# Kernel tuning notes

Hardware: AMD Instinct MI355X
Metric: run time of the kernel (lower is better)

## Reference

```python
import jax, jax.numpy as jnp
import numpy as np


def _adj(p):
    # p: [B,N,C] -> W = exp(-pairwise squared distance), fully dense (incl. self loops)
    sq = jnp.sum(p * p, axis=-1, keepdims=True)            # [B,N,1]
    d = sq - 2.0 * jnp.einsum('bnc,bmc->bnm', p, p) + jnp.swapaxes(sq, 1, 2)
    return jnp.exp(-d)


def _cheb_lap(W):
    # PyG ChebConv norm with sym normalization, lambda_max=2: L_hat = L - I = -D^{-1/2} W D^{-1/2}
    dinv = jax.lax.rsqrt(jnp.sum(W, axis=-1))              # [B,N]
    return -(dinv[:, :, None] * W * dinv[:, None, :])


def _reg_lap(W):
    # get_laplacian(sym) after remove_self_loops: L = I - D'^{-1/2} W' D'^{-1/2}, W' = W with zero diag
    N = W.shape[1]
    eye = jnp.eye(N, dtype=W.dtype)
    W0 = W * (1.0 - eye)
    dinv = jax.lax.rsqrt(jnp.sum(W0, axis=-1))
    return eye - dinv[:, :, None] * W0 * dinv[:, None, :]


def _cheb(x, Lhat, Wk, b):
    # Chebyshev recursion: Z0=x, Z1=L_hat x, Zk = 2 L_hat Z_{k-1} - Z_{k-2}
    # x: [B,N,Cin], Lhat: [B,N,N], Wk: [K,Cin,Cout]
    Z0 = x
    out = jnp.einsum('bni,io->bno', Z0, Wk[0])
    if Wk.shape[0] > 1:
        Z1 = jnp.einsum('bnm,bmi->bni', Lhat, x)
        out = out + jnp.einsum('bni,io->bno', Z1, Wk[1])
        for k in range(2, Wk.shape[0]):
            Z2 = 2.0 * jnp.einsum('bnm,bmi->bni', Lhat, Z1) - Z0
            out = out + jnp.einsum('bni,io->bno', Z2, Wk[k])
            Z0, Z1 = Z1, Z2
    return out + b


def _reg(out, L):
    # ||out^T L out||_F, block-diagonal L -> sum over batch blocks
    M = jnp.einsum('bnc,bnm,bmd->cd', out, L, out)
    return jnp.linalg.norm(M)


def setup_inputs() -> dict:
    key = jax.random.key(0)
    ks = jax.random.split(key, 16)
    B, N = 16, 1024
    s = 0.05
    return {
        'x': jax.random.normal(ks[0], (B, N, 6), dtype=jnp.float32),
        'batch': jnp.repeat(jnp.arange(B, dtype=jnp.int64 if jax.config.jax_enable_x64 else jnp.int32), N),
        'batch_size': B,
        'nr_points': N,
        'w1': jax.random.normal(ks[1], (6, 6, 128), dtype=jnp.float32) * s,
        'b1': jnp.zeros((128,), dtype=jnp.float32),
        'w2': jax.random.normal(ks[2], (5, 128, 512), dtype=jnp.float32) * s,
        'b2': jnp.zeros((512,), dtype=jnp.float32),
        'w3': jax.random.normal(ks[3], (3, 512, 1024), dtype=jnp.float32) * s,
        'b3': jnp.zeros((1024,), dtype=jnp.float32),
        'fw1': jax.random.normal(ks[4], (1024, 512), dtype=jnp.float32) * s,
        'fb1': jnp.zeros((512,), dtype=jnp.float32),
        'fw2': jax.random.normal(ks[5], (512, 128), dtype=jnp.float32) * s,
        'fb2': jnp.zeros((128,), dtype=jnp.float32),
        'fw3': jax.random.normal(ks[6], (128, 10), dtype=jnp.float32) * s,
        'fb3': jnp.zeros((10,), dtype=jnp.float32),
    }


def reference(x, batch, batch_size, nr_points, w1, b1, w2, b2, w3, b3,
              fw1, fb1, fw2, fb2, fw3, fb3):
    sg = jax.lax.stop_gradient
    # reshape of x happens inside torch.no_grad -> input to conv1 is detached
    h = sg(x)
    W1 = sg(_adj(x))
    out = jax.nn.relu(_cheb(h, _cheb_lap(W1), w1, b1))            # [B,N,128]
    r1 = sg(_reg(out, _reg_lap(W1)))
    W2 = sg(_adj(out))
    out = jax.nn.relu(_cheb(out, sg(_cheb_lap(W2)), w2, b2))      # [B,N,512]
    r2 = sg(_reg(out, _reg_lap(W2)))
    W3 = sg(_adj(out))
    out = jax.nn.relu(_cheb(out, sg(_cheb_lap(W3)), w3, b3))      # [B,N,1024]
    r3 = sg(_reg(out, _reg_lap(W3)))
    pooled = jnp.max(out, axis=1)                                  # MaxPool1d over points
    h = jax.nn.relu(pooled @ fw1 + fb1)
    h = jax.nn.relu(h @ fw2 + fb2)
    logits = h @ fw3 + fb3
    return logits, r1, r2, r3
```

## Files before the change

kernel.cpp:

```cpp
#include <hip/hip_runtime.h>

#define BB 16
#define NN 1024
#define LDT 16384

typedef float4 f4;
typedef __attribute__((ext_vector_type(8))) short bf16x8;
typedef __attribute__((ext_vector_type(4))) float f32x4;

__device__ __forceinline__ unsigned f2b1(float f) {
    unsigned u = __builtin_bit_cast(unsigned, f);
    return (u + 0x7fffu + ((u >> 16) & 1u)) >> 16;
}
__device__ __forceinline__ float b2f1(unsigned s) {
    unsigned u = (s & 0xffffu) << 16;
    return __builtin_bit_cast(float, u);
}

#define SW(r, k) ((r) * 64 + ((k) ^ (((((r) & 7) ^ (((r) >> 3) & 7))) << 3)))

__device__ __forceinline__ void gload16(const unsigned short* g, short* l) {
    __builtin_amdgcn_global_load_lds(
        (const __attribute__((address_space(1))) unsigned int*)g,
        (__attribute__((address_space(3))) unsigned int*)l, 16, 0, 0);
}

__device__ __forceinline__ float wave_sum(float v) {
    #pragma unroll
    for (int m = 32; m >= 1; m >>= 1) v += __shfl_xor(v, m);
    return v;
}
__device__ __forceinline__ float wave_max(float v) {
    #pragma unroll
    for (int m = 32; m >= 1; m >>= 1) v = fmaxf(v, __shfl_xor(v, m));
    return v;
}

__device__ __forceinline__ void stage_tr(short* T, const unsigned short* src,
                                         size_t col_base, int c0, int Cvalid, int tid) {
    #pragma unroll
    for (int n = 0; n < 2; n++) {
        int q = n * 256 + tid;
        int p = q >> 4, h = q & 15;
        int cg = c0 + 2 * p;
        uint4 r0 = make_uint4(0, 0, 0, 0), r1 = make_uint4(0, 0, 0, 0);
        if (cg < Cvalid)     r0 = *(const uint4*)&src[(size_t)cg * LDT + col_base + 8 * h];
        if (cg + 1 < Cvalid) r1 = *(const uint4*)&src[(size_t)(cg + 1) * LDT + col_base + 8 * h];
        const unsigned* a0 = (const unsigned*)&r0;
        const unsigned* a1 = (const unsigned*)&r1;
        #pragma unroll
        for (int e = 0; e < 8; e++) {
            unsigned lo = (e & 1) ? (a0[e >> 1] >> 16) : (a0[e >> 1] & 0xffffu);
            unsigned hi = (e & 1) ? (a1[e >> 1] >> 16) : (a1[e >> 1] & 0xffffu);
            int r = 8 * h + e;
            *(unsigned*)&T[SW(r, 2 * p)] = lo | (hi << 16);
        }
    }
}

__global__ void xt_prep_kernel(const float* __restrict__ x, short* __restrict__ xh,
                               short* __restrict__ xl) {
    int m = blockIdx.x * 256 + threadIdx.x;
    #pragma unroll
    for (int c = 0; c < 8; c++) {
        float v = (c < 6) ? x[(size_t)m * 6 + c] : 0.f;
        unsigned h = f2b1(v);
        unsigned l = f2b1(v - b2f1(h));
        xh[(size_t)c * LDT + m] = (short)h;
        xl[(size_t)c * LDT + m] = (short)l;
    }
}

__global__ void wtt_prep_kernel(const float* __restrict__ Wk, short* __restrict__ WtT,
                                int Kp64, int KpValid, int CpadM1, int shift, int Cin, int Cout) {
    int idx = blockIdx.x * 256 + threadIdx.x;
    if (idx >= Cout * Kp64) return;
    int co = idx / Kp64, kk = idx - co * Kp64;
    int c = kk & CpadM1;
    float val = 0.f;
    if (kk < KpValid && c < Cin)
        val = Wk[((size_t)(kk >> shift) * Cin + c) * Cout + co];
    WtT[(size_t)co * Kp64 + kk] = (short)f2b1(val);
}

__global__ void wtrans_kernel(const float* __restrict__ Wt, float* __restrict__ WtT,
                              int K, int O) {
    int idx = blockIdx.x * 256 + threadIdx.x;
    if (idx >= K * O) return;
    int o = idx / K, k = idx - o * K;
    WtT[idx] = Wt[(size_t)k * O + o];
}

__global__ void scale_sc_kernel(const short* __restrict__ src, const float* __restrict__ coeff,
                                short* __restrict__ dst, int total8) {
    int q = blockIdx.x * 256 + threadIdx.x;
    if (q >= total8) return;
    size_t base = (size_t)q * 8;
    int m8 = (int)(base & (LDT - 1));
    uint4 v = *(const uint4*)&((const unsigned short*)src)[base];
    f4 c0 = *(const f4*)&coeff[m8];
    f4 c1 = *(const f4*)&coeff[m8 + 4];
    const float* cp0 = (const float*)&c0;
    const float* cp1 = (const float*)&c1;
    unsigned* vp = (unsigned*)&v;
    #pragma unroll
    for (int e = 0; e < 4; e++) {
        float se0 = (e < 2) ? cp0[2 * e] : cp1[2 * e - 4];
        float se1 = (e < 2) ? cp0[2 * e + 1] : cp1[2 * e - 3];
        vp[e] = f2b1(b2f1(vp[e]) * se0) | (f2b1(b2f1(vp[e] >> 16) * se1) << 16);
    }
    *(uint4*)&((unsigned short*)dst)[base] = v;
}

__global__ __launch_bounds__(256)
void xpose_kernel(const short* __restrict__ H, const short* __restrict__ L,
                  int Cvalid, int CR, short* __restrict__ XRh, short* __restrict__ XRl) {
    __shared__ short Th[128 * 64], Tl[128 * 64];
    int tid = threadIdx.x;
    int m0 = blockIdx.x * 128, c0 = blockIdx.y * 64;
    stage_tr(Th, (const unsigned short*)H, m0, c0, Cvalid, tid);
    stage_tr(Tl, (const unsigned short*)L, m0, c0, Cvalid, tid);
    __syncthreads();
    #pragma unroll
    for (int n = 0; n < 4; n++) {
        int q = n * 256 + tid;
        int r = q >> 3, j = q & 7;
        int g = (r & 7) ^ ((r >> 3) & 7);
        *(uint4*)&XRh[(size_t)(m0 + r) * CR + c0 + 8 * j] = *(const uint4*)&Th[r * 64 + 8 * (j ^ g)];
        *(uint4*)&XRl[(size_t)(m0 + r) * CR + c0 + 8 * j] = *(const uint4*)&Tl[r * 64 + 8 * (j ^ g)];
    }
}

__global__ void sqt_part_kernel(const short* __restrict__ H, const short* __restrict__ L,
                                int C, float* __restrict__ dst) {
    int m = blockIdx.x * 256 + threadIdx.x;
    int cb = blockIdx.y * 128;
    int ce = min(cb + 128, C);
    const unsigned short* Hp = (const unsigned short*)H;
    const unsigned short* Lp = (const unsigned short*)L;
    float s = 0.f;
    for (int c = cb; c < ce; c++) {
        float v = b2f1(Hp[(size_t)c * LDT + m]) + b2f1(Lp[(size_t)c * LDT + m]);
        s += v * v;
    }
    dst[(size_t)blockIdx.y * LDT + m] = s;
}
__global__ void sqt_red_kernel(const float* __restrict__ part, int NC, float* __restrict__ sq) {
    int m = blockIdx.x * 256 + threadIdx.x;
    float s = 0.f;
    for (int y = 0; y < NC; y++) s += part[(size_t)y * LDT + m];
    sq[m] = s;
}

__global__ __launch_bounds__(256)
void adj_mfma_kernel(const short* __restrict__ XRh, const short* __restrict__ XRl,
                     int ck64, int CR, const float* __restrict__ sq,
                     short* __restrict__ Wb, float* __restrict__ Wpart,
                     float* __restrict__ diagW) {
    __shared__ short Ah[128 * 64], Al[128 * 64], Bh[128 * 64], Bl[128 * 64];
    __shared__ float jpart[128][2];
    int tid = threadIdx.x, lane = tid & 63, w = tid >> 6;
    int wj = w >> 1, wi = w & 1;
    int b = blockIdx.z, i0 = blockIdx.x * 128, j0 = blockIdx.y * 128;
    size_t bo = (size_t)b * NN;
    f32x4 acc[4][4] = {};
    const unsigned short* Hp = (const unsigned short*)XRh;
    const unsigned short* Lp = (const unsigned short*)XRl;
    int rr = lane >> 3, jj = lane & 7;
    size_t offI[4], offJ[4];
    #pragma unroll
    for (int m = 0; m < 4; m++) {
        int s = w + m * 4;
        int jc = jj ^ rr ^ (s & 7);
        offI[m] = (size_t)(bo + i0 + 8 * s + rr) * CR + 8 * jc;
        offJ[m] = (size_t)(bo + j0 + 8 * s + rr) * CR + 8 * jc;
    }
    for (int t = 0; t < ck64; t++) {
        int c0 = t * 64;
        #pragma unroll
        for (int m = 0; m < 4; m++) {
            int s512 = (w + m * 4) * 512;
            gload16(Hp + offI[m] + c0, Ah + s512);
            gload16(Lp + offI[m] + c0, Al + s512);
            gload16(Hp + offJ[m] + c0, Bh + s512);
            gload16(Lp + offJ[m] + c0, Bl + s512);
        }
        __syncthreads();
        int la = lane & 15;
        #pragma unroll
        for (int ks = 0; ks < 2; ks++) {
            int kb = ks * 32 + (lane >> 4) * 8;
            bf16x8 jh[4], jl[4], ih[4], il[4];
            #pragma unroll
            for (int f = 0; f < 4; f++) {
                int jr = wj * 64 + f * 16 + la;
                jh[f] = *(const bf16x8*)&Bh[SW(jr, kb)];
                jl[f] = *(const bf16x8*)&Bl[SW(jr, kb)];
                int ir = wi * 64 + f * 16 + la;
                ih[f] = *(const bf16x8*)&Ah[SW(ir, kb)];
                il[f] = *(const bf16x8*)&Al[SW(ir, kb)];
            }
            #pragma unroll
            for (int fq = 0; fq < 4; fq++)
                #pragma unroll
                for (int fi = 0; fi < 4; fi++) {
                    acc[fq][fi] = __builtin_amdgcn_mfma_f32_16x16x32_bf16(jh[fq], ih[fi], acc[fq][fi], 0, 0, 0);
                    acc[fq][fi] = __builtin_amdgcn_mfma_f32_16x16x32_bf16(jh[fq], il[fi], acc[fq][fi], 0, 0, 0);
                    acc[fq][fi] = __builtin_amdgcn_mfma_f32_16x16x32_bf16(jl[fq], ih[fi], acc[fq][fi], 0, 0, 0);
                }
        }
        __syncthreads();
    }
    const float* sqb = sq + bo;
    unsigned short* Wout = (unsigned short*)Wb + bo * NN;
    float si_[4];
    int iloc[4];
    #pragma unroll
    for (int fi = 0; fi < 4; fi++) {
        iloc[fi] = i0 + wi * 64 + fi * 16 + (lane & 15);
        si_[fi] = sqb[iloc[fi]];
    }
    #pragma unroll
    for (int fq = 0; fq < 4; fq++) {
        int jb = j0 + wj * 64 + fq * 16 + (lane >> 4) * 4;
        #pragma unroll
        for (int r = 0; r < 4; r++) {
            int j = jb + r;
            float sj = sqb[j];
            float p = 0.f;
            #pragma unroll
            for (int fi = 0; fi < 4; fi++) {
                float val = __expf(2.f * ((const float*)&acc[fq][fi])[r] - si_[fi] - sj);
                Wout[(size_t)j * NN + iloc[fi]] = (unsigned short)f2b1(val);
                if (iloc[fi] == j) diagW[bo + j] = val;
                else p += val;
            }
            p += __shfl_xor(p, 1); p += __shfl_xor(p, 2);
            p += __shfl_xor(p, 4); p += __shfl_xor(p, 8);
            if ((lane & 15) == 0)
                jpart[wj * 64 + fq * 16 + (lane >> 4) * 4 + r][wi] = p;
        }
    }
    __syncthreads();
    if (tid < 128)
        Wpart[(size_t)blockIdx.x * (BB * NN) + bo + j0 + tid] = jpart[tid][0] + jpart[tid][1];
}

__global__ void reduce_prep_kernel(const float* __restrict__ Wpart, const float* __restrict__ diagW,
                                   float* dinv, float* dinvP, float* cA1, float* cA2, float* cAV) {
    int idx = blockIdx.x * 256 + threadIdx.x;
    float s = 0.f;
    #pragma unroll
    for (int x = 0; x < 8; x++) s += Wpart[(size_t)x * (BB * NN) + idx];
    float d = diagW[idx];
    float dv = rsqrtf(s + d);
    float dp = rsqrtf(s);
    dinv[idx] = dv; dinvP[idx] = dp;
    cA1[idx] = -dv; cA2[idx] = -2.f * dv; cAV[idx] = -dp;
}

template<bool HAS_PREV, bool SKIP_DIAG, bool WRITE_SC>
__global__ __launch_bounds__(512)
void wgemm2_kernel(const short* __restrict__ W, const short* __restrict__ Bsc,
                   const float* __restrict__ cAvec, float prevSign,
                   const short* __restrict__ PrevT, const float* __restrict__ scVec,
                   short* __restrict__ DstT, short* __restrict__ DstSc, int Cvalid) {
    __shared__ short As[128 * 64], Bs[128 * 64];
    int tid = threadIdx.x, lane = tid & 63, w = tid >> 6;
    int wcc = w >> 2, wii = w & 3;
    int b = blockIdx.z, i0 = blockIdx.x * 128, c0 = blockIdx.y * 128;
    size_t bo = (size_t)b * NN;
    const unsigned short* Wp = (const unsigned short*)W + bo * NN;
    const unsigned short* Bp = (const unsigned short*)Bsc;
    int rr = lane >> 3, jj = lane & 7;
    int sA = w, sB = w + 8;
    int jc = jj ^ rr ^ (w & 7);
    const unsigned short* aR0 = Wp + (size_t)(i0 + 8 * sA + rr) * NN + 8 * jc;
    const unsigned short* aR1 = Wp + (size_t)(i0 + 8 * sB + rr) * NN + 8 * jc;
    const unsigned short* bR0 = Bp + (size_t)(c0 + 8 * sA + rr) * LDT + bo + 8 * jc;
    const unsigned short* bR1 = Bp + (size_t)(c0 + 8 * sB + rr) * LDT + bo + 8 * jc;
    short* aL0 = As + sA * 512; short* aL1 = As + sB * 512;
    short* bL0 = Bs + sA * 512; short* bL1 = Bs + sB * 512;
    f32x4 acc[4][2] = {};
    for (int k0 = 0; k0 < NN; k0 += 64) {
        gload16(aR0 + k0, aL0);
        gload16(aR1 + k0, aL1);
        gload16(bR0 + k0, bL0);
        gload16(bR1 + k0, bL1);
        __syncthreads();
        if (SKIP_DIAG) {
            if (k0 == i0 || k0 == i0 + 64) {
                if (tid < 64) As[SW((k0 - i0) + tid, tid)] = 0;
                __syncthreads();
            }
        }
        int la = lane & 15;
        #pragma unroll
        for (int ks = 0; ks < 2; ks++) {
            int kb = ks * 32 + (lane >> 4) * 8;
            bf16x8 ac[4], bi[2];
            #pragma unroll
            for (int f = 0; f < 4; f++) ac[f] = *(const bf16x8*)&Bs[SW(wcc * 64 + f * 16 + la, kb)];
            #pragma unroll
            for (int f = 0; f < 2; f++) bi[f] = *(const bf16x8*)&As[SW(wii * 32 + f * 16 + la, kb)];
            #pragma unroll
            for (int fq = 0; fq < 4; fq++)
                #pragma unroll
                for (int fi = 0; fi < 2; fi++)
                    acc[fq][fi] = __builtin_amdgcn_mfma_f32_16x16x32_bf16(ac[fq], bi[fi], acc[fq][fi], 0, 0, 0);
        }
        __syncthreads();
    }
    const unsigned short* Pp = (const unsigned short*)PrevT;
    unsigned short* Dp = (unsigned short*)DstT;
    unsigned short* Sp = (unsigned short*)DstSc;
    #pragma unroll
    for (int fi = 0; fi < 2; fi++) {
        int i = i0 + wii * 32 + fi * 16 + (lane & 15);
        float ca = cAvec[bo + i];
        float sc = WRITE_SC ? scVec[bo + i] : 0.f;
        #pragma unroll
        for (int fq = 0; fq < 4; fq++) {
            int cb = c0 + wcc * 64 + fq * 16 + (lane >> 4) * 4;
            const float* av = (const float*)&acc[fq][fi];
            #pragma unroll
            for (int r = 0; r < 4; r++) {
                int c = cb + r;
                if (c < Cvalid) {
                    float v = ca * av[r];
                    if (HAS_PREV) v += prevSign * b2f1(Pp[(size_t)c * LDT + bo + i]);
                    Dp[(size_t)c * LDT + bo + i] = (unsigned short)f2b1(v);
                    if (WRITE_SC) Sp[(size_t)c * LDT + bo + i] = (unsigned short)f2b1(v * sc);
                }
            }
        }
    }
}

__global__ __launch_bounds__(512)
void fgemm_mfma_kernel(const short* __restrict__ A0T, const short* __restrict__ ZrT,
                       const short* __restrict__ WtT, int Kp64, int KpValid, int Cpad,
                       const float* __restrict__ bias,
                       short* __restrict__ OutH, short* __restrict__ OutL) {
    __shared__ short As[128 * 64], Bs[128 * 64];
    int tid = threadIdx.x, lane = tid & 63, w = tid >> 6;
    int wco = w >> 2, wm = w & 3;
    int m0 = blockIdx.x * 128, co0 = blockIdx.y * 128;
    const unsigned short* A0 = (const unsigned short*)A0T;
    const unsigned short* Zr = (const unsigned short*)ZrT;
    const unsigned short* Wt = (const unsigned short*)WtT;
    f32x4 acc[4][2] = {};
    for (int kk0 = 0; kk0 < Kp64; kk0 += 64) {
        {
            int p = tid >> 4, h = tid & 15;
            int kg0 = kk0 + 2 * p;
            uint4 r0 = make_uint4(0, 0, 0, 0), r1 = make_uint4(0, 0, 0, 0);
            if (kg0 < KpValid) {
                const unsigned short* s0 = (kg0 < Cpad) ? (A0 + (size_t)kg0 * LDT)
                                                        : (Zr + (size_t)(kg0 - Cpad) * LDT);
                r0 = *(const uint4*)&s0[m0 + 8 * h];
            }
            if (kg0 + 1 < KpValid) {
                int kg1 = kg0 + 1;
                const unsigned short* s1 = (kg1 < Cpad) ? (A0 + (size_t)kg1 * LDT)
                                                        : (Zr + (size_t)(kg1 - Cpad) * LDT);
                r1 = *(const uint4*)&s1[m0 + 8 * h];
            }
            const unsigned* a0 = (const unsigned*)&r0;
            const unsigned* a1 = (const unsigned*)&r1;
            #pragma unroll
            for (int e = 0; e < 8; e++) {
                unsigned lo = (e & 1) ? (a0[e >> 1] >> 16) : (a0[e >> 1] & 0xffffu);
                unsigned hi = (e & 1) ? (a1[e >> 1] >> 16) : (a1[e >> 1] & 0xffffu);
                *(unsigned*)&As[SW(8 * h + e, 2 * p)] = lo | (hi << 16);
            }
        }
        #pragma unroll
        for (int n = 0; n < 2; n++) {
            int q = n * 512 + tid;
            int r = q >> 3, k8 = (q & 7) * 8;
            uint4 v = *(const uint4*)&Wt[(size_t)(co0 + r) * Kp64 + kk0 + k8];
            *(uint4*)&Bs[SW(r, k8)] = v;
        }
        __syncthreads();
        int la = lane & 15;
        #pragma unroll
        for (int ks = 0; ks < 2; ks++) {
            int kb = ks * 32 + (lane >> 4) * 8;
            bf16x8 ac[4], bm[2];
            #pragma unroll
            for (int f = 0; f < 4; f++) ac[f] = *(const bf16x8*)&Bs[SW(wco * 64 + f * 16 + la, kb)];
            #pragma unroll
            for (int f = 0; f < 2; f++) bm[f] = *(const bf16x8*)&As[SW(wm * 32 + f * 16 + la, kb)];
            #pragma unroll
            for (int fq = 0; fq < 4; fq++)
                #pragma unroll
                for (int fi = 0; fi < 2; fi++)
                    acc[fq][fi] = __builtin_amdgcn_mfma_f32_16x16x32_bf16(ac[fq], bm[fi], acc[fq][fi], 0, 0, 0);
        }
        __syncthreads();
    }
    unsigned short* OH = (unsigned short*)OutH;
    unsigned short* OL = (unsigned short*)OutL;
    #pragma unroll
    for (int fi = 0; fi < 2; fi++) {
        int m = m0 + wm * 32 + fi * 16 + (lane & 15);
        #pragma unroll
        for (int fq = 0; fq < 4; fq++) {
            int cb = co0 + wco * 64 + fq * 16 + (lane >> 4) * 4;
            const float* av = (const float*)&acc[fq][fi];
            #pragma unroll
            for (int r = 0; r < 4; r++) {
                int co = cb + r;
                float v = av[r] + bias[co];
                v = v > 0.f ? v : 0.f;
                unsigned ph = f2b1(v);
                unsigned pl = f2b1(v - b2f1(ph));
                OH[(size_t)co * LDT + m] = (unsigned short)ph;
                OL[(size_t)co * LDT + m] = (unsigned short)pl;
            }
        }
    }
}

__global__ __launch_bounds__(256)
void mgemm_mfma_kernel(const short* __restrict__ XT, const short* __restrict__ VT,
                       float* __restrict__ Mpart, int Cout, int kChunk) {
    __shared__ short As[128 * 64], Bs[128 * 64];
    int tid = threadIdx.x, lane = tid & 63, w = tid >> 6;
    int wcj = w >> 1, wci = w & 1;
    int ci0 = blockIdx.x * 128, cj0 = blockIdx.y * 128;
    int kStart = blockIdx.z * kChunk;
    const unsigned short* Xp = (const unsigned short*)XT + (size_t)ci0 * LDT;
    const unsigned short* Vp = (const unsigned short*)VT + (size_t)cj0 * LDT;
    int rr = lane >> 3, jj = lane & 7;
    const unsigned short* aB[4];
    const unsigned short* bB[4];
    short* aL[4]; short* bL[4];
    #pragma unroll
    for (int n = 0; n < 4; n++) {
        int s = w + n * 4;
        int jc = jj ^ rr ^ (s & 7);
        aB[n] = Xp + (size_t)(8 * s + rr) * LDT + 8 * jc;
        bB[n] = Vp + (size_t)(8 * s + rr) * LDT + 8 * jc;
        aL[n] = As + s * 512; bL[n] = Bs + s * 512;
    }
    f32x4 acc[4][4] = {};
    for (int k0 = kStart; k0 < kStart + kChunk; k0 += 64) {
        #pragma unroll
        for (int n = 0; n < 4; n++) {
            gload16(aB[n] + k0, aL[n]);
            gload16(bB[n] + k0, bL[n]);
        }
        __syncthreads();
        int la = lane & 15;
        #pragma unroll
        for (int ks = 0; ks < 2; ks++) {
            int kb = ks * 32 + (lane >> 4) * 8;
            bf16x8 aj[4], bi[4];
            #pragma unroll
            for (int f = 0; f < 4; f++) {
                aj[f] = *(const bf16x8*)&Bs[SW(wcj * 64 + f * 16 + la, kb)];
                bi[f] = *(const bf16x8*)&As[SW(wci * 64 + f * 16 + la, kb)];
            }
            #pragma unroll
            for (int fq = 0; fq < 4; fq++)
                #pragma unroll
                for (int fi = 0; fi < 4; fi++)
                    acc[fq][fi] = __builtin_amdgcn_mfma_f32_16x16x32_bf16(aj[fq], bi[fi], acc[fq][fi], 0, 0, 0);
        }
        __syncthreads();
    }
    float* pt = Mpart + (size_t)blockIdx.z * Cout * Cout;
    #pragma unroll
    for (int fq = 0; fq < 4; fq++) {
        int cjb = cj0 + wcj * 64 + fq * 16 + (lane >> 4) * 4;
        #pragma unroll
        for (int fi = 0; fi < 4; fi++) {
            int ci = ci0 + wci * 64 + fi * 16 + (lane & 15);
            const float* av = (const float*)&acc[fq][fi];
            #pragma unroll
            for (int r = 0; r < 4; r++)
                pt[(size_t)(cjb + r) * Cout + ci] = av[r];
        }
    }
}

__global__ void fro1_kernel(const float* __restrict__ part, int nElem, int splitk,
                            float* __restrict__ blockSS) {
    int tid = threadIdx.x;
    float ss = 0.f;
    for (int idx = blockIdx.x * 256 + tid; idx < nElem; idx += 1024 * 256) {
        float s = 0.f;
        for (int z = 0; z < splitk; z++) s += part[(size_t)z * nElem + idx];
        ss += s * s;
    }
    __shared__ float red[256];
    red[tid] = ss; __syncthreads();
    for (int m = 128; m >= 1; m >>= 1) { if (tid < m) red[tid] += red[tid + m]; __syncthreads(); }
    if (tid == 0) blockSS[blockIdx.x] = red[0];
}
__global__ void fro2_kernel(const float* __restrict__ blockSS, float* __restrict__ outp) {
    int tid = threadIdx.x;
    float s = 0.f;
    for (int i = tid; i < 1024; i += 256) s += blockSS[i];
    __shared__ float red[256];
    red[tid] = s; __syncthreads();
    for (int m = 128; m >= 1; m >>= 1) { if (tid < m) red[tid] += red[tid + m]; __syncthreads(); }
    if (tid == 0) *outp = sqrtf(red[0]);
}

__global__ void pool_kernel(const short* __restrict__ H, const short* __restrict__ L,
                            float* __restrict__ out) {
    int wave = threadIdx.x >> 6, lane = threadIdx.x & 63;
    int r = blockIdx.x * 4 + wave;
    int co = r >> 4, b = r & 15;
    const unsigned short* h = (const unsigned short*)H + (size_t)co * LDT + b * NN;
    const unsigned short* l = (const unsigned short*)L + (size_t)co * LDT + b * NN;
    float m = -1e30f;
    #pragma unroll
    for (int it = 0; it < 2; it++) {
        int n8 = (it * 64 + lane) * 8;
        uint4 vh = *(const uint4*)&h[n8];
        uint4 vl = *(const uint4*)&l[n8];
        const unsigned* hp = (const unsigned*)&vh;
        const unsigned* lp = (const unsigned*)&vl;
        #pragma unroll
        for (int e = 0; e < 4; e++) {
            m = fmaxf(m, b2f1(hp[e]) + b2f1(lp[e]));
            m = fmaxf(m, b2f1(hp[e] >> 16) + b2f1(lp[e] >> 16));
        }
    }
    m = wave_max(m);
    if (lane == 0) out[b * 1024 + co] = m;
}

__global__ void fc_kernel(const float* __restrict__ in, const float* __restrict__ WtT,
                          const float* __restrict__ bias, float* __restrict__ out,
                          int K, int O, int doRelu) {
    int wave = threadIdx.x >> 6, lane = threadIdx.x & 63;
    int idx = blockIdx.x * 4 + wave;
    if (idx >= 16 * O) return;
    int b = idx / O, o = idx - b * O;
    const float* ib = in + (size_t)b * K;
    const float* wr = WtT + (size_t)o * K;
    float s = 0.f;
    for (int k = lane * 4; k < K; k += 256) {
        f4 a = *(const f4*)&ib[k];
        f4 wv = *(const f4*)&wr[k];
        s += a.x * wv.x + a.y * wv.y + a.z * wv.z + a.w * wv.w;
    }
    s = wave_sum(s);
    if (lane == 0) {
        s += bias[o];
        if (doRelu) s = fmaxf(s, 0.f);
        out[(size_t)b * O + o] = s;
    }
}

extern "C" void kernel_launch(void* const* d_in, const int* in_sizes, int n_in,
                              void* d_out, int out_size, void* d_ws, size_t ws_size,
                              hipStream_t stream) {
    const float* x   = (const float*)d_in[0];
    const float* w1  = (const float*)d_in[4];
    const float* b1  = (const float*)d_in[5];
    const float* w2  = (const float*)d_in[6];
    const float* b2  = (const float*)d_in[7];
    const float* w3  = (const float*)d_in[8];
    const float* b3  = (const float*)d_in[9];
    const float* fw1 = (const float*)d_in[10];
    const float* fb1 = (const float*)d_in[11];
    const float* fw2 = (const float*)d_in[12];
    const float* fb2 = (const float*)d_in[13];
    const float* fw3 = (const float*)d_in[14];
    const float* fb3 = (const float*)d_in[15];
    float* out = (float*)d_out;

    char* ws = (char*)d_ws;
    size_t off = 0;
    auto alloc = [&](size_t bytes) -> void* {
        void* p = ws + off; off += (bytes + 255) & ~(size_t)255; return p;
    };
    short* Wbuf = (short*)alloc((size_t)BB * NN * NN * 2);
    short* Zbuf = (short*)alloc((size_t)1024 * LDT * 2);
    short* ZSc  = (short*)alloc((size_t)1024 * LDT * 2);
    short* Z0Sc = (short*)alloc((size_t)512 * LDT * 2);
    short* XRh  = (short*)alloc((size_t)512 * LDT * 2);
    short* XRl  = (short*)alloc((size_t)512 * LDT * 2);
    short* o1H  = (short*)alloc((size_t)128 * LDT * 2);
    short* o1L  = (short*)alloc((size_t)128 * LDT * 2);
    short* o2H  = (short*)alloc((size_t)512 * LDT * 2);
    short* o2L  = (short*)alloc((size_t)512 * LDT * 2);
    short* o3H  = (short*)alloc((size_t)1024 * LDT * 2);
    short* o3L  = (short*)alloc((size_t)1024 * LDT * 2);
    short* xTh  = (short*)alloc((size_t)8 * LDT * 2);
    short* xTl  = (short*)alloc((size_t)8 * LDT * 2);
    short* WtT  = (short*)alloc((size_t)1024 * 1536 * 2);
    float* fwT1 = (float*)alloc((size_t)512 * 1024 * 4);
    float* fwT2 = (float*)alloc((size_t)128 * 512 * 4);
    float* fwT3 = (float*)alloc((size_t)10 * 128 * 4);
    float* sqpart = (float*)alloc((size_t)8 * LDT * 4);
    float* Wpart  = (float*)alloc((size_t)8 * BB * NN * 4);
    float* diagW  = (float*)alloc(BB * NN * 4);
    float* sq    = (float*)alloc(BB * NN * 4);
    float* dinv  = (float*)alloc(BB * NN * 4);
    float* dinvP = (float*)alloc(BB * NN * 4);
    float* cA1   = (float*)alloc(BB * NN * 4);
    float* cA2   = (float*)alloc(BB * NN * 4);
    float* cAV   = (float*)alloc(BB * NN * 4);
    float* pooled= (float*)alloc(BB * 1024 * 4);
    float* h1    = (float*)alloc(BB * 512 * 4);
    float* h2    = (float*)alloc(BB * 128 * 4);
    float* blockSS = (float*)alloc(1024 * 4);
    float* Mpart = (float*)Wbuf;
    (void)ws_size; (void)in_sizes; (void)n_in; (void)out_size;

    struct Layer {
        const short *XTh, *XTl;
        int C, K, Cpad, shift, Kp64, KpValid, Cout, splitk, rIdx;
        const float *Wk, *bk;
        short *OutH, *OutL;
    };
    Layer L[3] = {
        { xTh, xTl, 8,   6, 8,   3, 64,   48,   128,  64, 160, w1, b1, o1H, o1L },
        { o1H, o1L, 128, 5, 128, 7, 640,  640,  512,  32, 161, w2, b2, o2H, o2L },
        { o2H, o2L, 512, 3, 512, 9, 1536, 1536, 1024, 8,  162, w3, b3, o3H, o3L },
    };

    xt_prep_kernel<<<LDT / 256, 256, 0, stream>>>(x, xTh, xTl);
    wtrans_kernel<<<(1024 * 512 + 255) / 256, 256, 0, stream>>>(fw1, fwT1, 1024, 512);
    wtrans_kernel<<<(512 * 128 + 255) / 256, 256, 0, stream>>>(fw2, fwT2, 512, 128);
    wtrans_kernel<<<(128 * 10 + 255) / 256, 256, 0, stream>>>(fw3, fwT3, 128, 10);

    for (int l = 0; l < 3; l++) {
        const Layer& P = L[l];
        int NC = (P.C + 127) / 128;
        int CR = (P.Cpad < 64) ? 64 : P.Cpad;
        wtt_prep_kernel<<<(P.Cout * P.Kp64 + 255) / 256, 256, 0, stream>>>(
            P.Wk, WtT, P.Kp64, P.KpValid, P.Cpad - 1, P.shift, (l == 0) ? 6 : P.C, P.Cout);
        sqt_part_kernel<<<dim3(LDT / 256, NC), 256, 0, stream>>>(P.XTh, P.XTl, P.C, sqpart);
        sqt_red_kernel<<<LDT / 256, 256, 0, stream>>>(sqpart, NC, sq);
        xpose_kernel<<<dim3(LDT / 128, CR / 64), 256, 0, stream>>>(
            P.XTh, P.XTl, P.Cpad, CR, XRh, XRl);
        adj_mfma_kernel<<<dim3(8, 8, BB), 256, 0, stream>>>(XRh, XRl, CR / 64, CR, sq,
                                                            Wbuf, Wpart, diagW);
        reduce_prep_kernel<<<BB * NN / 256, 256, 0, stream>>>(Wpart, diagW, dinv, dinvP, cA1, cA2, cAV);

        scale_sc_kernel<<<(P.Cpad * LDT / 8 + 255) / 256, 256, 0, stream>>>(
            P.XTh, dinv, Z0Sc, P.Cpad * LDT / 8);

        int cT = (P.Cpad + 127) / 128;
        auto sliceR = [&](int k) -> short* { return Zbuf + (size_t)(k - 1) * P.Cpad * LDT; };
        auto sliceS = [&](int k) -> short* { return ZSc  + (size_t)(k - 1) * P.Cpad * LDT; };
        if (P.K > 2)
            wgemm2_kernel<false, false, true><<<dim3(8, cT, BB), 512, 0, stream>>>(
                Wbuf, Z0Sc, cA1, 0.f, (const short*)nullptr, dinv, sliceR(1), sliceS(1), P.Cpad);
        else
            wgemm2_kernel<false, false, false><<<dim3(8, cT, BB), 512, 0, stream>>>(
                Wbuf, Z0Sc, cA1, 0.f, (const short*)nullptr, dinv, sliceR(1), (short*)nullptr, P.Cpad);
        for (int k = 2; k < P.K; k++) {
            const short* prevT = (k == 2) ? P.XTh : sliceR(k - 2);
            if (k < P.K - 1)
                wgemm2_kernel<true, false, true><<<dim3(8, cT, BB), 512, 0, stream>>>(
                    Wbuf, sliceS(k - 1), cA2, -1.f, prevT, dinv, sliceR(k), sliceS(k), P.Cpad);
            else
                wgemm2_kernel<true, false, false><<<dim3(8, cT, BB), 512, 0, stream>>>(
                    Wbuf, sliceS(k - 1), cA2, -1.f, prevT, dinv, sliceR(k), (short*)nullptr, P.Cpad);
        }
        fgemm_mfma_kernel<<<dim3(LDT / 128, P.Cout / 128), 512, 0, stream>>>(
            P.XTh, Zbuf, WtT, P.Kp64, P.KpValid, P.Cpad, P.bk, P.OutH, P.OutL);
        scale_sc_kernel<<<(P.Cout * LDT / 8 + 255) / 256, 256, 0, stream>>>(
            P.OutH, dinvP, ZSc, P.Cout * LDT / 8);
        wgemm2_kernel<true, true, false><<<dim3(8, P.Cout / 128, BB), 512, 0, stream>>>(
            Wbuf, ZSc, cAV, 1.f, P.OutH, dinvP, Zbuf, (short*)nullptr, P.Cout);
        int kChunk = LDT / P.splitk;
        mgemm_mfma_kernel<<<dim3(P.Cout / 128, P.Cout / 128, P.splitk), 256, 0, stream>>>(
            P.OutH, Zbuf, Mpart, P.Cout, kChunk);
        fro1_kernel<<<1024, 256, 0, stream>>>(Mpart, P.Cout * P.Cout, P.splitk, blockSS);
        fro2_kernel<<<1, 256, 0, stream>>>(blockSS, out + P.rIdx);
    }
    pool_kernel<<<16384 / 4, 256, 0, stream>>>(o3H, o3L, pooled);
    fc_kernel<<<(16 * 512 + 3) / 4, 256, 0, stream>>>(pooled, fwT1, fb1, h1, 1024, 512, 1);
    fc_kernel<<<(16 * 128 + 3) / 4, 256, 0, stream>>>(h1, fwT2, fb2, h2, 512, 128, 1);
    fc_kernel<<<(16 * 10 + 3) / 4, 256, 0, stream>>>(h2, fwT3, fb3, out, 128, 10, 0);
}
```

Before: 962.8 us.

## Use 64-row W tiles for narrow layers and prefetch A in fgemm

Adds an XB template parameter to the Laplacian GEMM kernel so layers with at most 128 channels use 64-row tiles. This doubles the block count where the grid was small (8x1x16) and should improve occupancy. Separately, fgemm now loads its weight tile asynchronously into LDS via global_load_lds and prefetches the next A tile into registers during compute, overlapping global loads with MFMA work. The costs are more re-reads of the B operand with smaller tiles and extra register pressure from the prefetch.

```diff
diff --git a/kernel.cpp b/kernel.cpp
--- a/kernel.cpp
+++ b/kernel.cpp
@@ -259,37 +259,38 @@
     cA1[idx] = -dv; cA2[idx] = -2.f * dv; cAV[idx] = -dp;
 }
 
-template<bool HAS_PREV, bool SKIP_DIAG, bool WRITE_SC>
+template<bool HAS_PREV, bool SKIP_DIAG, bool WRITE_SC, int XB>
 __global__ __launch_bounds__(512)
 void wgemm2_kernel(const short* __restrict__ W, const short* __restrict__ Bsc,
                    const float* __restrict__ cAvec, float prevSign,
                    const short* __restrict__ PrevT, const float* __restrict__ scVec,
                    short* __restrict__ DstT, short* __restrict__ DstSc, int Cvalid) {
-    __shared__ short As[128 * 64], Bs[128 * 64];
+    __shared__ short As[XB * 64], Bs[128 * 64];
+    constexpr int NFI = XB / 64;
     int tid = threadIdx.x, lane = tid & 63, w = tid >> 6;
     int wcc = w >> 2, wii = w & 3;
-    int b = blockIdx.z, i0 = blockIdx.x * 128, c0 = blockIdx.y * 128;
+    int b = blockIdx.z, i0 = blockIdx.x * XB, c0 = blockIdx.y * 128;
     size_t bo = (size_t)b * NN;
     const unsigned short* Wp = (const unsigned short*)W + bo * NN;
     const unsigned short* Bp = (const unsigned short*)Bsc;
     int rr = lane >> 3, jj = lane & 7;
-    int sA = w, sB = w + 8;
     int jc = jj ^ rr ^ (w & 7);
-    const unsigned short* aR0 = Wp + (size_t)(i0 + 8 * sA + rr) * NN + 8 * jc;
-    const unsigned short* aR1 = Wp + (size_t)(i0 + 8 * sB + rr) * NN + 8 * jc;
-    const unsigned short* bR0 = Bp + (size_t)(c0 + 8 * sA + rr) * LDT + bo + 8 * jc;
-    const unsigned short* bR1 = Bp + (size_t)(c0 + 8 * sB + rr) * LDT + bo + 8 * jc;
-    short* aL0 = As + sA * 512; short* aL1 = As + sB * 512;
-    short* bL0 = Bs + sA * 512; short* bL1 = Bs + sB * 512;
-    f32x4 acc[4][2] = {};
+    const unsigned short* aR0 = Wp + (size_t)(i0 + 8 * w + rr) * NN + 8 * jc;
+    const unsigned short* aR1 = Wp + (size_t)(i0 + 8 * ((XB == 128) ? w + 8 : w) + rr) * NN + 8 * jc;
+    const unsigned short* bR0 = Bp + (size_t)(c0 + 8 * w + rr) * LDT + bo + 8 * jc;
+    const unsigned short* bR1 = Bp + (size_t)(c0 + 8 * (w + 8) + rr) * LDT + bo + 8 * jc;
+    short* aL0 = As + w * 512;
+    short* aL1 = As + ((XB == 128) ? w + 8 : w) * 512;
+    short* bL0 = Bs + w * 512; short* bL1 = Bs + (w + 8) * 512;
+    f32x4 acc[4][NFI] = {};
     for (int k0 = 0; k0 < NN; k0 += 64) {
         gload16(aR0 + k0, aL0);
-        gload16(aR1 + k0, aL1);
+        if (XB == 128) gload16(aR1 + k0, aL1);
         gload16(bR0 + k0, bL0);
         gload16(bR1 + k0, bL1);
         __syncthreads();
         if (SKIP_DIAG) {
-            if (k0 == i0 || k0 == i0 + 64) {
+            if (k0 >= i0 && k0 < i0 + XB) {
                 if (tid < 64) As[SW((k0 - i0) + tid, tid)] = 0;
                 __syncthreads();
             }
@@ -298,15 +299,15 @@
         #pragma unroll
         for (int ks = 0; ks < 2; ks++) {
             int kb = ks * 32 + (lane >> 4) * 8;
-            bf16x8 ac[4], bi[2];
+            bf16x8 ac[4], bi[NFI];
             #pragma unroll
             for (int f = 0; f < 4; f++) ac[f] = *(const bf16x8*)&Bs[SW(wcc * 64 + f * 16 + la, kb)];
             #pragma unroll
-            for (int f = 0; f < 2; f++) bi[f] = *(const bf16x8*)&As[SW(wii * 32 + f * 16 + la, kb)];
+            for (int f = 0; f < NFI; f++) bi[f] = *(const bf16x8*)&As[SW(wii * (XB / 4) + f * 16 + la, kb)];
             #pragma unroll
             for (int fq = 0; fq < 4; fq++)
                 #pragma unroll
-                for (int fi = 0; fi < 2; fi++)
+                for (int fi = 0; fi < NFI; fi++)
                     acc[fq][fi] = __builtin_amdgcn_mfma_f32_16x16x32_bf16(ac[fq], bi[fi], acc[fq][fi], 0, 0, 0);
         }
         __syncthreads();
@@ -315,8 +316,8 @@
     unsigned short* Dp = (unsigned short*)DstT;
     unsigned short* Sp = (unsigned short*)DstSc;
     #pragma unroll
-    for (int fi = 0; fi < 2; fi++) {
-        int i = i0 + wii * 32 + fi * 16 + (lane & 15);
+    for (int fi = 0; fi < NFI; fi++) {
+        int i = i0 + wii * (XB / 4) + fi * 16 + (lane & 15);
         float ca = cAvec[bo + i];
         float sc = WRITE_SC ? scVec[bo + i] : 0.f;
         #pragma unroll
@@ -349,25 +350,34 @@
     const unsigned short* A0 = (const unsigned short*)A0T;
     const unsigned short* Zr = (const unsigned short*)ZrT;
     const unsigned short* Wt = (const unsigned short*)WtT;
+    int rr = lane >> 3, jj = lane & 7;
+    int jcB = jj ^ rr ^ (w & 7);
+    const unsigned short* bB0 = Wt + (size_t)(co0 + 8 * w + rr) * Kp64 + 8 * jcB;
+    const unsigned short* bB1 = Wt + (size_t)(co0 + 8 * (w + 8) + rr) * Kp64 + 8 * jcB;
+    short* bL0 = Bs + w * 512; short* bL1 = Bs + (w + 8) * 512;
+    int p = tid >> 4, h = tid & 15;
+    uint4 ra0, ra1;
+    auto loadA = [&](int kk0) {
+        int kg0 = kk0 + 2 * p;
+        ra0 = make_uint4(0, 0, 0, 0); ra1 = make_uint4(0, 0, 0, 0);
+        if (kg0 < KpValid) {
+            const unsigned short* s0 = (kg0 < Cpad) ? (A0 + (size_t)kg0 * LDT)
+                                                    : (Zr + (size_t)(kg0 - Cpad) * LDT);
+            ra0 = *(const uint4*)&s0[m0 + 8 * h];
+        }
+        if (kg0 + 1 < KpValid) {
+            int kg1 = kg0 + 1;
+            const unsigned short* s1 = (kg1 < Cpad) ? (A0 + (size_t)kg1 * LDT)
+                                                    : (Zr + (size_t)(kg1 - Cpad) * LDT);
+            ra1 = *(const uint4*)&s1[m0 + 8 * h];
+        }
+    };
     f32x4 acc[4][2] = {};
+    loadA(0);
     for (int kk0 = 0; kk0 < Kp64; kk0 += 64) {
         {
-            int p = tid >> 4, h = tid & 15;
-            int kg0 = kk0 + 2 * p;
-            uint4 r0 = make_uint4(0, 0, 0, 0), r1 = make_uint4(0, 0, 0, 0);
-            if (kg0 < KpValid) {
-                const unsigned short* s0 = (kg0 < Cpad) ? (A0 + (size_t)kg0 * LDT)
-                                                        : (Zr + (size_t)(kg0 - Cpad) * LDT);
-                r0 = *(const uint4*)&s0[m0 + 8 * h];
-            }
-            if (kg0 + 1 < KpValid) {
-                int kg1 = kg0 + 1;
-                const unsigned short* s1 = (kg1 < Cpad) ? (A0 + (size_t)kg1 * LDT)
-                                                        : (Zr + (size_t)(kg1 - Cpad) * LDT);
-                r1 = *(const uint4*)&s1[m0 + 8 * h];
-            }
-            const unsigned* a0 = (const unsigned*)&r0;
-            const unsigned* a1 = (const unsigned*)&r1;
+            const unsigned* a0 = (const unsigned*)&ra0;
+            const unsigned* a1 = (const unsigned*)&ra1;
             #pragma unroll
             for (int e = 0; e < 8; e++) {
                 unsigned lo = (e & 1) ? (a0[e >> 1] >> 16) : (a0[e >> 1] & 0xffffu);
@@ -375,14 +385,10 @@
                 *(unsigned*)&As[SW(8 * h + e, 2 * p)] = lo | (hi << 16);
             }
         }
-        #pragma unroll
-        for (int n = 0; n < 2; n++) {
-            int q = n * 512 + tid;
-            int r = q >> 3, k8 = (q & 7) * 8;
-            uint4 v = *(const uint4*)&Wt[(size_t)(co0 + r) * Kp64 + kk0 + k8];
-            *(uint4*)&Bs[SW(r, k8)] = v;
-        }
+        gload16(bB0 + kk0, bL0);
+        gload16(bB1 + kk0, bL1);
         __syncthreads();
+        if (kk0 + 64 < Kp64) loadA(kk0 + 64);
         int la = lane & 15;
         #pragma unroll
         for (int ks = 0; ks < 2; ks++) {
@@ -650,29 +656,45 @@
             P.XTh, dinv, Z0Sc, P.Cpad * LDT / 8);
 
         int cT = (P.Cpad + 127) / 128;
+        bool sm = (P.Cpad <= 128);
         auto sliceR = [&](int k) -> short* { return Zbuf + (size_t)(k - 1) * P.Cpad * LDT; };
         auto sliceS = [&](int k) -> short* { return ZSc  + (size_t)(k - 1) * P.Cpad * LDT; };
-        if (P.K > 2)
-            wgemm2_kernel<false, false, true><<<dim3(8, cT, BB), 512, 0, stream>>>(
-                Wbuf, Z0Sc, cA1, 0.f, (const short*)nullptr, dinv, sliceR(1), sliceS(1), P.Cpad);
-        else
-            wgemm2_kernel<false, false, false><<<dim3(8, cT, BB), 512, 0, stream>>>(
-                Wbuf, Z0Sc, cA1, 0.f, (const short*)nullptr, dinv, sliceR(1), (short*)nullptr, P.Cpad);
+        if (P.K > 2) {
+            if (sm) wgemm2_kernel<false, false, true, 64><<<dim3(NN / 64, cT, BB), 512, 0, stream>>>(
+                        Wbuf, Z0Sc, cA1, 0.f, (const short*)nullptr, dinv, sliceR(1), sliceS(1), P.Cpad);
+            else    wgemm2_kernel<false, false, true, 128><<<dim3(NN / 128, cT, BB), 512, 0, stream>>>(
+                        Wbuf, Z0Sc, cA1, 0.f, (const short*)nullptr, dinv, sliceR(1), sliceS(1), P.Cpad);
+        } else {
+            if (sm) wgemm2_kernel<false, false, false, 64><<<dim3(NN / 64, cT, BB), 512, 0, stream>>>(
+                        Wbuf, Z0Sc, cA1, 0.f, (const short*)nullptr, dinv, sliceR(1), (short*)nullptr, P.Cpad);
+            else    wgemm2_kernel<false, false, false, 128><<<dim3(NN / 128, cT, BB), 512, 0, stream>>>(
+                        Wbuf, Z0Sc, cA1, 0.f, (const short*)nullptr, dinv, sliceR(1), (short*)nullptr, P.Cpad);
+        }
         for (int k = 2; k < P.K; k++) {
             const short* prevT = (k == 2) ? P.XTh : sliceR(k - 2);
-            if (k < P.K - 1)
-                wgemm2_kernel<true, false, true><<<dim3(8, cT, BB), 512, 0, stream>>>(
-                    Wbuf, sliceS(k - 1), cA2, -1.f, prevT, dinv, sliceR(k), sliceS(k), P.Cpad);
-            else
-                wgemm2_kernel<true, false, false><<<dim3(8, cT, BB), 512, 0, stream>>>(
-                    Wbuf, sliceS(k - 1), cA2, -1.f, prevT, dinv, sliceR(k), (short*)nullptr, P.Cpad);
+            if (k < P.K - 1) {
+                if (sm) wgemm2_kernel<true, false, true, 64><<<dim3(NN / 64, cT, BB), 512, 0, stream>>>(
+                            Wbuf, sliceS(k - 1), cA2, -1.f, prevT, dinv, sliceR(k), sliceS(k), P.Cpad);
+                else    wgemm2_kernel<true, false, true, 128><<<dim3(NN / 128, cT, BB), 512, 0, stream>>>(
+                            Wbuf, sliceS(k - 1), cA2, -1.f, prevT, dinv, sliceR(k), sliceS(k), P.Cpad);
+            } else {
+                if (sm) wgemm2_kernel<true, false, false, 64><<<dim3(NN / 64, cT, BB), 512, 0, stream>>>(
+                            Wbuf, sliceS(k - 1), cA2, -1.f, prevT, dinv, sliceR(k), (short*)nullptr, P.Cpad);
+                else    wgemm2_kernel<true, false, false, 128><<<dim3(NN / 128, cT, BB), 512, 0, stream>>>(
+                            Wbuf, sliceS(k - 1), cA2, -1.f, prevT, dinv, sliceR(k), (short*)nullptr, P.Cpad);
+            }
         }
         fgemm_mfma_kernel<<<dim3(LDT / 128, P.Cout / 128), 512, 0, stream>>>(
             P.XTh, Zbuf, WtT, P.Kp64, P.KpValid, P.Cpad, P.bk, P.OutH, P.OutL);
         scale_sc_kernel<<<(P.Cout * LDT / 8 + 255) / 256, 256, 0, stream>>>(
             P.OutH, dinvP, ZSc, P.Cout * LDT / 8);
-        wgemm2_kernel<true, true, false><<<dim3(8, P.Cout / 128, BB), 512, 0, stream>>>(
-            Wbuf, ZSc, cAV, 1.f, P.OutH, dinvP, Zbuf, (short*)nullptr, P.Cout);
+        int cTV = P.Cout / 128;
+        if (P.Cout <= 128)
+            wgemm2_kernel<true, true, false, 64><<<dim3(NN / 64, cTV, BB), 512, 0, stream>>>(
+                Wbuf, ZSc, cAV, 1.f, P.OutH, dinvP, Zbuf, (short*)nullptr, P.Cout);
+        else
+            wgemm2_kernel<true, true, false, 128><<<dim3(NN / 128, cTV, BB), 512, 0, stream>>>(
+                Wbuf, ZSc, cAV, 1.f, P.OutH, dinvP, Zbuf, (short*)nullptr, P.Cout);
         int kChunk = LDT / P.splitk;
         mgemm_mfma_kernel<<<dim3(P.Cout / 128, P.Cout / 128, P.splitk), 256, 0, stream>>>(
             P.OutH, Zbuf, Mpart, P.Cout, kChunk);
```

Measured after the change: 920.0 us (median of 2 runs). -4.4%, faster.
